# Optimization experiments

Measured on AMD Instinct MI355X. Metric: run time of the kernel, lower is better.

The kernel has to match this reference:

```python
import jax, jax.numpy as jnp
import numpy as np

L, H, C, HS, V, BS = 4, 8, 512, 64, 32000, 2048  # layers, heads, n_embd, head_size, vocab, block_size
B, T = 2, 2048


def _ln(x, g, b, eps=1e-5):
    m = jnp.mean(x, axis=-1, keepdims=True)
    v = jnp.var(x, axis=-1, keepdims=True)
    return (x - m) * jax.lax.rsqrt(v + eps) * g + b


def setup_inputs() -> dict:
    key = jax.random.key(0)
    ks = jax.random.split(key, 12)
    s = 0.02
    f = jnp.float32
    return {
        "idx": jax.random.randint(ks[0], (B, T), 0, V),
        "tok_emb": jax.random.normal(ks[1], (V, C), f) * s,
        "pos_emb": jax.random.normal(ks[2], (BS, C), f) * s,
        "ln1_g": jnp.ones((L, C), f), "ln1_b": jnp.zeros((L, C), f),
        "wq": jax.random.normal(ks[3], (L, H, C, HS), f) * s,
        "wk": jax.random.normal(ks[4], (L, H, C, HS), f) * s,
        "wv": jax.random.normal(ks[5], (L, H, C, HS), f) * s,
        "proj_w": jax.random.normal(ks[6], (L, C, C), f) * s,
        "proj_b": jnp.zeros((L, C), f),
        "ln2_g": jnp.ones((L, C), f), "ln2_b": jnp.zeros((L, C), f),
        "ff_w1": jax.random.normal(ks[7], (L, C, 4 * C), f) * s,
        "ff_b1": jnp.zeros((L, 4 * C), f),
        "ff_w2": jax.random.normal(ks[8], (L, 4 * C, C), f) * s,
        "ff_b2": jnp.zeros((L, C), f),
        "ffln_g": jnp.ones((L, C), f), "ffln_b": jnp.zeros((L, C), f),
        "lm_w": jax.random.normal(ks[9], (C, V), f) * s,
        "lm_b": jnp.zeros((V,), f),
    }


def reference(idx, tok_emb, pos_emb, ln1_g, ln1_b, wq, wk, wv, proj_w, proj_b,
              ln2_g, ln2_b, ff_w1, ff_b1, ff_w2, ff_b2, ffln_g, ffln_b, lm_w, lm_b):
    Tn = idx.shape[1]
    x = tok_emb[idx] + pos_emb[:Tn]  # [B,T,C]
    causal = jnp.tril(jnp.ones((Tn, Tn), bool))
    for l in range(L):
        h = _ln(x, ln1_g[l], ln1_b[l])
        q = jnp.einsum('btc,hcd->bhtd', h, wq[l])
        k = jnp.einsum('btc,hcd->bhtd', h, wk[l])
        v = jnp.einsum('btc,hcd->bhtd', h, wv[l])
        # NOTE: original module does NOT scale by 1/sqrt(head_size)
        wei = jnp.einsum('bhtd,bhsd->bhts', q, k)
        wei = jnp.where(causal, wei, -jnp.inf)
        wei = jax.nn.softmax(wei, axis=-1)
        att = jnp.einsum('bhts,bhsd->bhtd', wei, v)  # [B,H,T,HS]
        att = att.transpose(0, 2, 1, 3).reshape(x.shape[0], Tn, C)
        x = x + att @ proj_w[l].T + proj_b[l]
        h2 = _ln(x, ln2_g[l], ln2_b[l])
        ff = jax.nn.relu(h2 @ ff_w1[l] + ff_b1[l]) @ ff_w2[l] + ff_b2[l]
        ff = _ln(ff, ffln_g[l], ffln_b[l])  # FeedForward has trailing LayerNorm
        x = x + ff
    logits = x @ lm_w + lm_b  # [B,T,V]
    return logits
```

## Files before the change

kernel.cpp:

```cpp
#include <hip/hip_runtime.h>
#include <math.h>

#define NLAYER 4
#define NH     8
#define CDIM   512
#define HS     64
#define VOCAB  32000
#define BB     2
#define TT     2048
#define MROWS  (BB*TT)
#define QKVW   (3*CDIM)
#define NHEADS (BB*NH)

typedef __attribute__((ext_vector_type(8))) short bf16x8;
typedef __attribute__((ext_vector_type(4))) float f32x4;

__device__ __forceinline__ unsigned short f2bf(float f) {
    unsigned int u = __float_as_uint(f);
    u += 0x7FFF + ((u >> 16) & 1);
    return (unsigned short)(u >> 16);
}

#define GLOAD16(g, l) __builtin_amdgcn_global_load_lds( \
    (const __attribute__((address_space(1))) void*)(g), \
    (__attribute__((address_space(3))) void*)(l), 16, 0, 0)

template<int FLAGS, bool OUTBF>
__global__ __launch_bounds__(256) void mfma_gemm(
    const unsigned short* __restrict__ A, int lda,
    const unsigned short* __restrict__ Bt, int ldb,
    const float* __restrict__ bias,
    void* __restrict__ Cout, int ldc,
    const float* __restrict__ resid,
    int K)
{
    __shared__ unsigned short As[128*64];
    __shared__ unsigned short Bs[128*64];
    const int tid = threadIdx.x;
    const int w = tid >> 6, l = tid & 63;
    const int wr = w >> 1, wc = w & 1;
    const long m0 = (long)blockIdx.y * 128;
    const long n0 = (long)blockIdx.x * 128;
    const int srow = l >> 3;
    const int scol = (l & 7) << 3;
    const unsigned short* Ab = A + m0*lda;
    const unsigned short* Bb = Bt + n0*ldb;
    const int fr = l & 15;
    const int fk = (l >> 4) << 3;

    f32x4 acc[4][4];
    #pragma unroll
    for (int m = 0; m < 4; m++)
        #pragma unroll
        for (int n = 0; n < 4; n++) acc[m][n] = (f32x4)0.0f;

    for (int k0 = 0; k0 < K; k0 += 64) {
        __syncthreads();
        #pragma unroll
        for (int i = 0; i < 4; i++) {
            int seg = w*4 + i;
            GLOAD16(Ab + (long)(seg*8 + srow)*lda + k0 + scol, As + seg*512);
            GLOAD16(Bb + (long)(seg*8 + srow)*ldb + k0 + scol, Bs + seg*512);
        }
        __syncthreads();
        #pragma unroll
        for (int kk = 0; kk < 2; kk++) {
            bf16x8 af[4], bf[4];
            #pragma unroll
            for (int m = 0; m < 4; m++)
                af[m] = *(const bf16x8*)&As[(wr*64 + m*16 + fr)*64 + kk*32 + fk];
            #pragma unroll
            for (int n = 0; n < 4; n++)
                bf[n] = *(const bf16x8*)&Bs[(wc*64 + n*16 + fr)*64 + kk*32 + fk];
            #pragma unroll
            for (int m = 0; m < 4; m++)
                #pragma unroll
                for (int n = 0; n < 4; n++)
                    acc[m][n] = __builtin_amdgcn_mfma_f32_16x16x32_bf16(
                        af[m], bf[n], acc[m][n], 0, 0, 0);
        }
    }

    const int rg = (l >> 4) << 2;
    #pragma unroll
    for (int n = 0; n < 4; n++) {
        long gn = n0 + wc*64 + n*16 + fr;
        float bv = (FLAGS & 1) ? bias[gn] : 0.f;
        #pragma unroll
        for (int m = 0; m < 4; m++) {
            #pragma unroll
            for (int r = 0; r < 4; r++) {
                long gm = m0 + wr*64 + m*16 + rg + r;
                float val = acc[m][n][r] + bv;
                if (FLAGS & 2) val = fmaxf(val, 0.f);
                if (FLAGS & 4) val += resid[gm*ldc + gn];
                if (OUTBF) ((unsigned short*)Cout)[gm*ldc + gn] = f2bf(val);
                else       ((float*)Cout)[gm*ldc + gn] = val;
            }
        }
    }
}

__global__ __launch_bounds__(256) void mfma_gemm_qkv(
    const unsigned short* __restrict__ A,
    const unsigned short* __restrict__ Bt,
    unsigned short* __restrict__ qh,
    unsigned short* __restrict__ kh,
    unsigned short* __restrict__ vt)
{
    __shared__ unsigned short As[128*64];
    __shared__ unsigned short Bs[128*64];
    const int tid = threadIdx.x;
    const int w = tid >> 6, l = tid & 63;
    const int wr = w >> 1, wc = w & 1;
    const long m0 = (long)blockIdx.y * 128;
    const long n0 = (long)blockIdx.x * 128;
    const int srow = l >> 3;
    const int scol = (l & 7) << 3;
    const unsigned short* Ab = A + m0*CDIM;
    const unsigned short* Bb = Bt + n0*CDIM;
    const int fr = l & 15;
    const int fk = (l >> 4) << 3;

    f32x4 acc[4][4];
    #pragma unroll
    for (int m = 0; m < 4; m++)
        #pragma unroll
        for (int n = 0; n < 4; n++) acc[m][n] = (f32x4)0.0f;

    for (int k0 = 0; k0 < CDIM; k0 += 64) {
        __syncthreads();
        #pragma unroll
        for (int i = 0; i < 4; i++) {
            int seg = w*4 + i;
            GLOAD16(Ab + (long)(seg*8 + srow)*CDIM + k0 + scol, As + seg*512);
            GLOAD16(Bb + (long)(seg*8 + srow)*CDIM + k0 + scol, Bs + seg*512);
        }
        __syncthreads();
        #pragma unroll
        for (int kk = 0; kk < 2; kk++) {
            bf16x8 af[4], bf[4];
            #pragma unroll
            for (int m = 0; m < 4; m++)
                af[m] = *(const bf16x8*)&As[(wr*64 + m*16 + fr)*64 + kk*32 + fk];
            #pragma unroll
            for (int n = 0; n < 4; n++)
                bf[n] = *(const bf16x8*)&Bs[(wc*64 + n*16 + fr)*64 + kk*32 + fk];
            #pragma unroll
            for (int m = 0; m < 4; m++)
                #pragma unroll
                for (int n = 0; n < 4; n++)
                    acc[m][n] = __builtin_amdgcn_mfma_f32_16x16x32_bf16(
                        af[m], bf[n], acc[m][n], 0, 0, 0);
        }
    }

    const int rg = (l >> 4) << 2;
    #pragma unroll
    for (int n = 0; n < 4; n++) {
        int gn = (int)(n0 + wc*64 + n*16 + fr);
        int which = gn >> 9, hh = (gn >> 6) & 7, d = gn & 63;
        #pragma unroll
        for (int m = 0; m < 4; m++) {
            #pragma unroll
            for (int r = 0; r < 4; r++) {
                int gm = (int)(m0 + wr*64 + m*16 + rg + r);
                int b = gm >> 11, t = gm & (TT-1);
                int head = b*NH + hh;
                unsigned short val = f2bf(acc[m][n][r]);
                if (which == 0)      qh[((long)head*TT + t)*HS + d] = val;
                else if (which == 1) kh[((long)head*TT + t)*HS + d] = val;
                else                 vt[((long)head*HS + d)*TT + t] = val;
            }
        }
    }
}

__global__ __launch_bounds__(256) void attn_part(
    const unsigned short* __restrict__ qh,
    const unsigned short* __restrict__ kh,
    const unsigned short* __restrict__ vt,
    float* __restrict__ oP, float* __restrict__ ml)
{
    __shared__ unsigned short Ks[2][64*64];
    __shared__ unsigned short Vts[2][64*64];
    __shared__ unsigned short Ps[4][32*72];
    const int tid = threadIdx.x;
    const int w = tid >> 6, l = tid & 63;
    const int fr = l & 15, g = l >> 4;
    const int head = blockIdx.y;
    const int sp = blockIdx.z;
    const int x = blockIdx.x;
    const int qt0 = x * 128;
    const int qw = qt0 + w*32;
    const unsigned short* Qb = qh + (long)head*TT*HS;
    const unsigned short* Kb = kh + (long)head*TT*HS;
    const unsigned short* Vb = vt + (long)head*HS*TT;

    bf16x8 aq[2][2];
    #pragma unroll
    for (int mt = 0; mt < 2; mt++)
        #pragma unroll
        for (int ks = 0; ks < 2; ks++)
            aq[mt][ks] = *(const bf16x8*)&Qb[(long)(qw + mt*16 + fr)*HS + ks*32 + g*8];

    f32x4 acc_o[2][4];
    float mrun[2][4], lsum[2][4];
    #pragma unroll
    for (int mt = 0; mt < 2; mt++) {
        #pragma unroll
        for (int r = 0; r < 4; r++) { mrun[mt][r] = -INFINITY; lsum[mt][r] = 0.f; }
        #pragma unroll
        for (int n = 0; n < 4; n++) acc_o[mt][n] = (f32x4)0.0f;
    }

    const int cbeg = sp * (x + 1);
    const int cend = cbeg + (x + 1);
    const int srow = l >> 3;
    const int scol = ((l & 7) ^ (srow & 7)) << 3;

    auto stage = [&](int c) {
        int buf = c & 1;
        int s0_ = c*64;
        #pragma unroll
        for (int i = 0; i < 2; i++) {
            int rb = i*32 + w*8;
            GLOAD16(Kb + (long)(s0_ + rb + srow)*HS + scol, &Ks[buf][rb*64]);
            GLOAD16(Vb + (long)(rb + srow)*TT + s0_ + scol, &Vts[buf][rb*64]);
        }
    };

    stage(cbeg);
    for (int c = cbeg; c < cend; c++) {
        const int s0 = c*64;
        const int buf = c & 1;
        __syncthreads();
        if (c + 1 < cend) stage(c+1);
        if (s0 > qw + 31) continue;

        bf16x8 bk[4][2];
        #pragma unroll
        for (int n = 0; n < 4; n++)
            #pragma unroll
            for (int ks = 0; ks < 2; ks++) {
                int row = n*16 + fr;
                int u = (ks*4 + g) ^ (row & 7);
                bk[n][ks] = *(const bf16x8*)&Ks[buf][row*64 + u*8];
            }
        f32x4 sc[2][4];
        #pragma unroll
        for (int mt = 0; mt < 2; mt++)
            #pragma unroll
            for (int n = 0; n < 4; n++) sc[mt][n] = (f32x4)0.0f;
        #pragma unroll
        for (int ks = 0; ks < 2; ks++)
            #pragma unroll
            for (int mt = 0; mt < 2; mt++)
                #pragma unroll
                for (int n = 0; n < 4; n++)
                    sc[mt][n] = __builtin_amdgcn_mfma_f32_16x16x32_bf16(
                        aq[mt][ks], bk[n][ks], sc[mt][n], 0, 0, 0);

        #pragma unroll
        for (int mt = 0; mt < 2; mt++) {
            #pragma unroll
            for (int r = 0; r < 4; r++) {
                int q = qw + mt*16 + g*4 + r;
                float rmax = -INFINITY;
                #pragma unroll
                for (int n = 0; n < 4; n++) {
                    float v = sc[mt][n][r];
                    v = (s0 + n*16 + fr <= q) ? v : -INFINITY;
                    sc[mt][n][r] = v;
                    rmax = fmaxf(rmax, v);
                }
                #pragma unroll
                for (int off = 8; off >= 1; off >>= 1)
                    rmax = fmaxf(rmax, __shfl_xor(rmax, off));
                float mnew = fmaxf(mrun[mt][r], rmax);
                float scale = __expf(mrun[mt][r] - mnew);
                float ps = 0.f;
                #pragma unroll
                for (int n = 0; n < 4; n++) {
                    float p = __expf(sc[mt][n][r] - mnew);
                    sc[mt][n][r] = p;
                    ps += p;
                }
                #pragma unroll
                for (int off = 8; off >= 1; off >>= 1)
                    ps += __shfl_xor(ps, off);
                lsum[mt][r] = lsum[mt][r]*scale + ps;
                mrun[mt][r] = mnew;
                #pragma unroll
                for (int n = 0; n < 4; n++) acc_o[mt][n][r] *= scale;
            }
        }

        #pragma unroll
        for (int mt = 0; mt < 2; mt++)
            #pragma unroll
            for (int n = 0; n < 4; n++)
                #pragma unroll
                for (int r = 0; r < 4; r++)
                    Ps[w][(mt*16 + g*4 + r)*72 + n*16 + fr] = f2bf(sc[mt][n][r]);

        bf16x8 ap[2][2], bv[4][2];
        #pragma unroll
        for (int mt = 0; mt < 2; mt++)
            #pragma unroll
            for (int ks = 0; ks < 2; ks++)
                ap[mt][ks] = *(const bf16x8*)&Ps[w][(mt*16 + fr)*72 + ks*32 + g*8];
        #pragma unroll
        for (int n = 0; n < 4; n++)
            #pragma unroll
            for (int ks = 0; ks < 2; ks++) {
                int row = n*16 + fr;
                int u = (ks*4 + g) ^ (row & 7);
                bv[n][ks] = *(const bf16x8*)&Vts[buf][row*64 + u*8];
            }
        #pragma unroll
        for (int ks = 0; ks < 2; ks++)
            #pragma unroll
            for (int mt = 0; mt < 2; mt++)
                #pragma unroll
                for (int n = 0; n < 4; n++)
                    acc_o[mt][n] = __builtin_amdgcn_mfma_f32_16x16x32_bf16(
                        ap[mt][ks], bv[n][ks], acc_o[mt][n], 0, 0, 0);
    }

    float* oB = oP + ((long)(head*2 + sp)*TT)*HS;
    float* mlB = ml + ((long)(head*2 + sp)*TT)*2;
    #pragma unroll
    for (int mt = 0; mt < 2; mt++) {
        #pragma unroll
        for (int n = 0; n < 4; n++)
            #pragma unroll
            for (int r = 0; r < 4; r++)
                oB[(long)(qw + mt*16 + g*4 + r)*HS + n*16 + fr] = acc_o[mt][n][r];
        if (fr == 0) {
            #pragma unroll
            for (int r = 0; r < 4; r++) {
                int t = qw + mt*16 + g*4 + r;
                mlB[t*2]     = mrun[mt][r];
                mlB[t*2 + 1] = lsum[mt][r];
            }
        }
    }
}

__global__ __launch_bounds__(256) void attn_combine(
    const float* __restrict__ oP, const float* __restrict__ ml,
    unsigned short* __restrict__ att)
{
    const int gid = blockIdx.x*4 + (threadIdx.x >> 6);
    const int lane = threadIdx.x & 63;
    const int head = gid >> 11, t = gid & (TT-1);
    const int b = head >> 3, hh = head & 7;
    const long i0 = (long)(head*2 + 0)*TT + t;
    const long i1 = (long)(head*2 + 1)*TT + t;
    const float m0 = ml[i0*2], l0 = ml[i0*2+1];
    const float m1 = ml[i1*2], l1 = ml[i1*2+1];
    const float M = fmaxf(m0, m1);
    const float e0 = __expf(m0 - M), e1 = __expf(m1 - M);
    const float L = l0*e0 + l1*e1;
    const float v = (oP[i0*HS + lane]*e0 + oP[i1*HS + lane]*e1) / L;
    att[((long)b*TT + t)*CDIM + hh*HS + lane] = f2bf(v);
}

__global__ __launch_bounds__(256) void transpose_cast(
    const float* __restrict__ in, unsigned short* __restrict__ out,
    int R, int Cn, long in_z1, long in_z2, long out_z1, long out_z2, int z2n)
{
    const int z = blockIdx.z;
    const int z1 = z / z2n, z2 = z % z2n;
    const float* ip = in + (long)z1*in_z1 + (long)z2*in_z2;
    unsigned short* op = out + (long)z1*out_z1 + (long)z2*out_z2;
    __shared__ float tile[32][33];
    const int tx = threadIdx.x & 31, ty = threadIdx.x >> 5;
    const long r0 = (long)blockIdx.y*32, c0 = (long)blockIdx.x*32;
    #pragma unroll
    for (int i = 0; i < 4; i++)
        tile[ty + i*8][tx] = ip[(r0 + ty + i*8)*Cn + c0 + tx];
    __syncthreads();
    #pragma unroll
    for (int i = 0; i < 4; i++)
        op[(c0 + ty + i*8)*R + r0 + tx] = f2bf(tile[tx][ty + i*8]);
}

__global__ __launch_bounds__(256) void cast_kernel(
    const float* __restrict__ in, unsigned short* __restrict__ out, long n)
{
    long i = ((long)blockIdx.x*256 + threadIdx.x) * 4;
    if (i >= n) return;
    float4 v = *(const float4*)(in + i);
    ushort4 u = make_ushort4(f2bf(v.x), f2bf(v.y), f2bf(v.z), f2bf(v.w));
    *(ushort4*)(out + i) = u;
}

__global__ void embed_kernel(const int* __restrict__ idx,
                             const float* __restrict__ tok,
                             const float* __restrict__ pos,
                             float* __restrict__ x)
{
    const int r = blockIdx.x;
    const int t = r & (TT-1);
    const long tr = idx[r];
    const float* te = tok + tr*CDIM;
    const float* pe = pos + (long)t*CDIM;
    float* xo = x + (long)r*CDIM;
    for (int c = threadIdx.x; c < CDIM; c += blockDim.x)
        xo[c] = te[c] + pe[c];
}

template<int MODE>
__global__ __launch_bounds__(256) void ln_kernel(
    const float* __restrict__ in, const float* __restrict__ g,
    const float* __restrict__ bb, void* __restrict__ outp,
    void* __restrict__ outp2)
{
    const int wave = threadIdx.x >> 6;
    const int lane = threadIdx.x & 63;
    const long r = (long)blockIdx.x*4 + wave;
    const float* xr = in + r*CDIM;
    float vals[8];
    float s = 0.f;
    #pragma unroll
    for (int i = 0; i < 8; i++) { vals[i] = xr[lane + i*64]; s += vals[i]; }
    #pragma unroll
    for (int o = 32; o >= 1; o >>= 1) s += __shfl_xor(s, o);
    const float mean = s * (1.f/CDIM);
    float vs = 0.f;
    #pragma unroll
    for (int i = 0; i < 8; i++) { float d = vals[i]-mean; vs += d*d; }
    #pragma unroll
    for (int o = 32; o >= 1; o >>= 1) vs += __shfl_xor(vs, o);
    const float rstd = rsqrtf(vs*(1.f/CDIM) + 1e-5f);
    #pragma unroll
    for (int i = 0; i < 8; i++) {
        int c = lane + i*64;
        float nv = (vals[i]-mean)*rstd*g[c] + bb[c];
        if (MODE == 1) {
            ((unsigned short*)outp)[r*CDIM + c] = f2bf(nv);
        } else {
            float s2 = ((float*)outp)[r*CDIM + c] + nv;
            ((float*)outp)[r*CDIM + c] = s2;
            if (MODE == 3) ((unsigned short*)outp2)[r*CDIM + c] = f2bf(s2);
        }
    }
}

extern "C" void kernel_launch(void* const* d_in, const int* in_sizes, int n_in,
                              void* d_out, int out_size, void* d_ws, size_t ws_size,
                              hipStream_t stream)
{
    const int*   idx   = (const int*)  d_in[0];
    const float* tok   = (const float*)d_in[1];
    const float* pos   = (const float*)d_in[2];
    const float* ln1g  = (const float*)d_in[3];
    const float* ln1b  = (const float*)d_in[4];
    const float* wq    = (const float*)d_in[5];
    const float* wk    = (const float*)d_in[6];
    const float* wv    = (const float*)d_in[7];
    const float* projw = (const float*)d_in[8];
    const float* projb = (const float*)d_in[9];
    const float* ln2g  = (const float*)d_in[10];
    const float* ln2b  = (const float*)d_in[11];
    const float* ffw1  = (const float*)d_in[12];
    const float* ffb1  = (const float*)d_in[13];
    const float* ffw2  = (const float*)d_in[14];
    const float* ffb2  = (const float*)d_in[15];
    const float* flng  = (const float*)d_in[16];
    const float* flnb  = (const float*)d_in[17];
    const float* lmw   = (const float*)d_in[18];
    const float* lmb   = (const float*)d_in[19];
    float* out = (float*)d_out;

    char* wp = (char*)d_ws;
    float* x  = (float*)wp;           wp += (size_t)MROWS*CDIM*4;
    float* ff = (float*)wp;           wp += (size_t)MROWS*CDIM*4;
    unsigned short* h     = (unsigned short*)wp; wp += (size_t)MROWS*CDIM*2;
    unsigned short* lmt   = (unsigned short*)wp; wp += (size_t)VOCAB*CDIM*2;
    unsigned short* ff1t  = (unsigned short*)wp; wp += (size_t)NLAYER*4*CDIM*CDIM*2;
    unsigned short* ff2t  = (unsigned short*)wp; wp += (size_t)NLAYER*4*CDIM*CDIM*2;
    unsigned short* qkvt  = (unsigned short*)wp; wp += (size_t)NLAYER*QKVW*CDIM*2;
    unsigned short* projc = (unsigned short*)wp; wp += (size_t)NLAYER*CDIM*CDIM*2;
    unsigned short* qh    = (unsigned short*)wp; wp += (size_t)NHEADS*TT*HS*2;
    unsigned short* kh    = (unsigned short*)wp; wp += (size_t)NHEADS*TT*HS*2;
    unsigned short* vt    = (unsigned short*)wp; wp += (size_t)NHEADS*TT*HS*2;

    unsigned short* f1  = (unsigned short*)d_out;
    unsigned short* att = f1 + (size_t)MROWS*4*CDIM;
    float* oP = (float*)(att + (size_t)MROWS*CDIM);
    float* ml = oP + (size_t)NHEADS*2*TT*HS;

    transpose_cast<<<dim3(VOCAB/32, CDIM/32, 1), 256, 0, stream>>>(
        lmw, lmt, CDIM, VOCAB, 0, 0, 0, 0, 1);
    transpose_cast<<<dim3(4*CDIM/32, CDIM/32, NLAYER), 256, 0, stream>>>(
        ffw1, ff1t, CDIM, 4*CDIM, (long)CDIM*4*CDIM, 0, (long)4*CDIM*CDIM, 0, 1);
    transpose_cast<<<dim3(CDIM/32, 4*CDIM/32, NLAYER), 256, 0, stream>>>(
        ffw2, ff2t, 4*CDIM, CDIM, (long)4*CDIM*CDIM, 0, (long)CDIM*4*CDIM, 0, 1);
    {
        const size_t QBLK = (size_t)CDIM * CDIM;
        transpose_cast<<<dim3(HS/32, CDIM/32, NLAYER*NH), 256, 0, stream>>>(
            wq, qkvt,            CDIM, HS,
            (long)NH*CDIM*HS, (long)CDIM*HS, (long)QKVW*CDIM, (long)HS*CDIM, NH);
        transpose_cast<<<dim3(HS/32, CDIM/32, NLAYER*NH), 256, 0, stream>>>(
            wk, qkvt + QBLK,     CDIM, HS,
            (long)NH*CDIM*HS, (long)CDIM*HS, (long)QKVW*CDIM, (long)HS*CDIM, NH);
        transpose_cast<<<dim3(HS/32, CDIM/32, NLAYER*NH), 256, 0, stream>>>(
            wv, qkvt + 2*QBLK,   CDIM, HS,
            (long)NH*CDIM*HS, (long)CDIM*HS, (long)QKVW*CDIM, (long)HS*CDIM, NH);
    }
    cast_kernel<<<(NLAYER*CDIM*CDIM/4 + 255)/256, 256, 0, stream>>>(
        projw, projc, (long)NLAYER*CDIM*CDIM);

    embed_kernel<<<MROWS, 256, 0, stream>>>(idx, tok, pos, x);

    for (int l = 0; l < NLAYER; l++) {
        const unsigned short* qkvt_l = qkvt + (size_t)l*QKVW*CDIM;
        const unsigned short* projc_l = projc + (size_t)l*CDIM*CDIM;
        const unsigned short* ff1t_l = ff1t + (size_t)l*4*CDIM*CDIM;
        const unsigned short* ff2t_l = ff2t + (size_t)l*4*CDIM*CDIM;

        ln_kernel<1><<<MROWS/4, 256, 0, stream>>>(x, ln1g + l*CDIM, ln1b + l*CDIM, h, nullptr);

        mfma_gemm_qkv<<<dim3(QKVW/128, MROWS/128), 256, 0, stream>>>(
            h, qkvt_l, qh, kh, vt);

        attn_part<<<dim3(TT/128, NHEADS, 2), 256, 0, stream>>>(qh, kh, vt, oP, ml);
        attn_combine<<<dim3(NHEADS*TT/4), 256, 0, stream>>>(oP, ml, att);

        mfma_gemm<5,false><<<dim3(CDIM/128, MROWS/128), 256, 0, stream>>>(
            att, CDIM, projc_l, CDIM, projb + l*CDIM, x, CDIM, x, CDIM);

        ln_kernel<1><<<MROWS/4, 256, 0, stream>>>(x, ln2g + l*CDIM, ln2b + l*CDIM, h, nullptr);

        mfma_gemm<3,true><<<dim3(4*CDIM/128, MROWS/128), 256, 0, stream>>>(
            h, CDIM, ff1t_l, CDIM, ffb1 + (size_t)l*4*CDIM, f1, 4*CDIM, nullptr, CDIM);

        mfma_gemm<1,false><<<dim3(CDIM/128, MROWS/128), 256, 0, stream>>>(
            f1, 4*CDIM, ff2t_l, 4*CDIM, ffb2 + l*CDIM, ff, CDIM, nullptr, 4*CDIM);

        if (l == NLAYER-1)
            ln_kernel<3><<<MROWS/4, 256, 0, stream>>>(ff, flng + l*CDIM, flnb + l*CDIM, x, h);
        else
            ln_kernel<2><<<MROWS/4, 256, 0, stream>>>(ff, flng + l*CDIM, flnb + l*CDIM, x, nullptr);
    }

    mfma_gemm<1,false><<<dim3(VOCAB/128, MROWS/128), 256, 0, stream>>>(
        h, CDIM, lmt, CDIM, lmb, out, VOCAB, nullptr, CDIM);
}
```

Measured before the change: 1.034 ms.

## Double-buffer GEMM LDS tiles with XOR swizzle, grouped LM-head tiling, nontemporal stores

The GEMM kernels now double-buffer the LDS tiles, so the next K-slice loads while MFMAs run on the current one. The LDS layout gets an XOR swizzle to cut bank conflicts. The LM-head GEMM uses a swizzled block order and nontemporal stores for its large fp32 logits output, aiming at better L2 reuse of weight tiles and less cache pollution. The attention split count is now a macro, and the combine kernel is generalized to loop over it. Double buffering doubles LDS use to 64KB per block, which may lower occupancy.

```diff
diff --git a/kernel.cpp b/kernel.cpp
--- a/kernel.cpp
+++ b/kernel.cpp
@@ -11,6 +11,7 @@
 #define MROWS  (BB*TT)
 #define QKVW   (3*CDIM)
 #define NHEADS (BB*NH)
+#define ASPLIT 2
 
 typedef __attribute__((ext_vector_type(8))) short bf16x8;
 typedef __attribute__((ext_vector_type(4))) float f32x4;
@@ -25,7 +26,9 @@
     (const __attribute__((address_space(1))) void*)(g), \
     (__attribute__((address_space(3))) void*)(l), 16, 0, 0)
 
-template<int FLAGS, bool OUTBF>
+#define SWZ(row, chunk) (((row)*64) + ((((chunk) ^ ((row)&7)))*8))
+
+template<int FLAGS, bool OUTBF, bool MSWIZ>
 __global__ __launch_bounds__(256) void mfma_gemm(
     const unsigned short* __restrict__ A, int lda,
     const unsigned short* __restrict__ Bt, int ldb,
@@ -34,19 +37,118 @@
     const float* __restrict__ resid,
     int K)
 {
-    __shared__ unsigned short As[128*64];
-    __shared__ unsigned short Bs[128*64];
+    __shared__ unsigned short As[2][128*64];
+    __shared__ unsigned short Bs[2][128*64];
+    const int tid = threadIdx.x;
+    const int w = tid >> 6, l = tid & 63;
+    const int wr = w >> 1, wc = w & 1;
+    long m0, n0;
+    if (MSWIZ) {
+        const int mt = gridDim.x;
+        const int flat = blockIdx.y * mt + blockIdx.x;
+        const int cpx = (mt * gridDim.y) >> 3;
+        const int swz = (flat & 7) * cpx + (flat >> 3);
+        m0 = (long)(swz % mt) * 128;
+        n0 = (long)(swz / mt) * 128;
+    } else {
+        m0 = (long)blockIdx.y * 128;
+        n0 = (long)blockIdx.x * 128;
+    }
+    const int srow = l >> 3;
+    const int scol = ((l & 7) ^ (srow & 7)) << 3;
+    const unsigned short* Ab = A + m0*lda;
+    const unsigned short* Bb = Bt + n0*ldb;
+    const int fr = l & 15;
+    const int g  = l >> 4;
+
+    f32x4 acc[4][4];
+    #pragma unroll
+    for (int m = 0; m < 4; m++)
+        #pragma unroll
+        for (int n = 0; n < 4; n++) acc[m][n] = (f32x4)0.0f;
+
+    auto stage = [&](int k0, int buf) {
+        #pragma unroll
+        for (int i = 0; i < 4; i++) {
+            int seg = w*4 + i;
+            GLOAD16(Ab + (long)(seg*8 + srow)*lda + k0 + scol, &As[buf][seg*512]);
+            GLOAD16(Bb + (long)(seg*8 + srow)*ldb + k0 + scol, &Bs[buf][seg*512]);
+        }
+    };
+
+    const int nk = K >> 6;
+    stage(0, 0);
+    for (int ks = 0; ks < nk; ks++) {
+        const int buf = ks & 1;
+        __syncthreads();
+        if (ks + 1 < nk) stage((ks+1) << 6, buf ^ 1);
+        #pragma unroll
+        for (int kk = 0; kk < 2; kk++) {
+            bf16x8 af[4], bf[4];
+            #pragma unroll
+            for (int m = 0; m < 4; m++) {
+                int row = wr*64 + m*16 + fr;
+                af[m] = *(const bf16x8*)&As[buf][SWZ(row, kk*4 + g)];
+            }
+            #pragma unroll
+            for (int n = 0; n < 4; n++) {
+                int row = wc*64 + n*16 + fr;
+                bf[n] = *(const bf16x8*)&Bs[buf][SWZ(row, kk*4 + g)];
+            }
+            #pragma unroll
+            for (int m = 0; m < 4; m++)
+                #pragma unroll
+                for (int n = 0; n < 4; n++)
+                    acc[m][n] = __builtin_amdgcn_mfma_f32_16x16x32_bf16(
+                        af[m], bf[n], acc[m][n], 0, 0, 0);
+        }
+    }
+
+    const int rg = g << 2;
+    #pragma unroll
+    for (int n = 0; n < 4; n++) {
+        long gn = n0 + wc*64 + n*16 + fr;
+        float bv = (FLAGS & 1) ? bias[gn] : 0.f;
+        #pragma unroll
+        for (int m = 0; m < 4; m++) {
+            #pragma unroll
+            for (int r = 0; r < 4; r++) {
+                long gm = m0 + wr*64 + m*16 + rg + r;
+                float val = acc[m][n][r] + bv;
+                if (FLAGS & 2) val = fmaxf(val, 0.f);
+                if (FLAGS & 4) val += resid[gm*ldc + gn];
+                if (OUTBF) {
+                    ((unsigned short*)Cout)[gm*ldc + gn] = f2bf(val);
+                } else if (FLAGS & 8) {
+                    __builtin_nontemporal_store(val, &((float*)Cout)[gm*ldc + gn]);
+                } else {
+                    ((float*)Cout)[gm*ldc + gn] = val;
+                }
+            }
+        }
+    }
+}
+
+__global__ __launch_bounds__(256) void mfma_gemm_qkv(
+    const unsigned short* __restrict__ A,
+    const unsigned short* __restrict__ Bt,
+    unsigned short* __restrict__ qh,
+    unsigned short* __restrict__ kh,
+    unsigned short* __restrict__ vt)
+{
+    __shared__ unsigned short As[2][128*64];
+    __shared__ unsigned short Bs[2][128*64];
     const int tid = threadIdx.x;
     const int w = tid >> 6, l = tid & 63;
     const int wr = w >> 1, wc = w & 1;
     const long m0 = (long)blockIdx.y * 128;
     const long n0 = (long)blockIdx.x * 128;
     const int srow = l >> 3;
-    const int scol = (l & 7) << 3;
-    const unsigned short* Ab = A + m0*lda;
-    const unsigned short* Bb = Bt + n0*ldb;
+    const int scol = ((l & 7) ^ (srow & 7)) << 3;
+    const unsigned short* Ab = A + m0*CDIM;
+    const unsigned short* Bb = Bt + n0*CDIM;
     const int fr = l & 15;
-    const int fk = (l >> 4) << 3;
+    const int g  = l >> 4;
 
     f32x4 acc[4][4];
     #pragma unroll
@@ -54,24 +156,34 @@
         #pragma unroll
         for (int n = 0; n < 4; n++) acc[m][n] = (f32x4)0.0f;
 
-    for (int k0 = 0; k0 < K; k0 += 64) {
-        __syncthreads();
+    auto stage = [&](int k0, int buf) {
         #pragma unroll
         for (int i = 0; i < 4; i++) {
             int seg = w*4 + i;
-            GLOAD16(Ab + (long)(seg*8 + srow)*lda + k0 + scol, As + seg*512);
-            GLOAD16(Bb + (long)(seg*8 + srow)*ldb + k0 + scol, Bs + seg*512);
-        }
+            GLOAD16(Ab + (long)(seg*8 + srow)*CDIM + k0 + scol, &As[buf][seg*512]);
+            GLOAD16(Bb + (long)(seg*8 + srow)*CDIM + k0 + scol, &Bs[buf][seg*512]);
+        }
+    };
+
+    const int nk = CDIM >> 6;
+    stage(0, 0);
+    for (int ks = 0; ks < nk; ks++) {
+        const int buf = ks & 1;
         __syncthreads();
+        if (ks + 1 < nk) stage((ks+1) << 6, buf ^ 1);
         #pragma unroll
         for (int kk = 0; kk < 2; kk++) {
             bf16x8 af[4], bf[4];
             #pragma unroll
-            for (int m = 0; m < 4; m++)
-                af[m] = *(const bf16x8*)&As[(wr*64 + m*16 + fr)*64 + kk*32 + fk];
-            #pragma unroll
-            for (int n = 0; n < 4; n++)
-                bf[n] = *(const bf16x8*)&Bs[(wc*64 + n*16 + fr)*64 + kk*32 + fk];
+            for (int m = 0; m < 4; m++) {
+                int row = wr*64 + m*16 + fr;
+                af[m] = *(const bf16x8*)&As[buf][SWZ(row, kk*4 + g)];
+            }
+            #pragma unroll
+            for (int n = 0; n < 4; n++) {
+                int row = wc*64 + n*16 + fr;
+                bf[n] = *(const bf16x8*)&Bs[buf][SWZ(row, kk*4 + g)];
+            }
             #pragma unroll
             for (int m = 0; m < 4; m++)
                 #pragma unroll
@@ -81,81 +193,7 @@
         }
     }
 
-    const int rg = (l >> 4) << 2;
-    #pragma unroll
-    for (int n = 0; n < 4; n++) {
-        long gn = n0 + wc*64 + n*16 + fr;
-        float bv = (FLAGS & 1) ? bias[gn] : 0.f;
-        #pragma unroll
-        for (int m = 0; m < 4; m++) {
-            #pragma unroll
-            for (int r = 0; r < 4; r++) {
-                long gm = m0 + wr*64 + m*16 + rg + r;
-                float val = acc[m][n][r] + bv;
-                if (FLAGS & 2) val = fmaxf(val, 0.f);
-                if (FLAGS & 4) val += resid[gm*ldc + gn];
-                if (OUTBF) ((unsigned short*)Cout)[gm*ldc + gn] = f2bf(val);
-                else       ((float*)Cout)[gm*ldc + gn] = val;
-            }
-        }
-    }
-}
-
-__global__ __launch_bounds__(256) void mfma_gemm_qkv(
-    const unsigned short* __restrict__ A,
-    const unsigned short* __restrict__ Bt,
-    unsigned short* __restrict__ qh,
-    unsigned short* __restrict__ kh,
-    unsigned short* __restrict__ vt)
-{
-    __shared__ unsigned short As[128*64];
-    __shared__ unsigned short Bs[128*64];
-    const int tid = threadIdx.x;
-    const int w = tid >> 6, l = tid & 63;
-    const int wr = w >> 1, wc = w & 1;
-    const long m0 = (long)blockIdx.y * 128;
-    const long n0 = (long)blockIdx.x * 128;
-    const int srow = l >> 3;
-    const int scol = (l & 7) << 3;
-    const unsigned short* Ab = A + m0*CDIM;
-    const unsigned short* Bb = Bt + n0*CDIM;
-    const int fr = l & 15;
-    const int fk = (l >> 4) << 3;
-
-    f32x4 acc[4][4];
-    #pragma unroll
-    for (int m = 0; m < 4; m++)
-        #pragma unroll
-        for (int n = 0; n < 4; n++) acc[m][n] = (f32x4)0.0f;
-
-    for (int k0 = 0; k0 < CDIM; k0 += 64) {
-        __syncthreads();
-        #pragma unroll
-        for (int i = 0; i < 4; i++) {
-            int seg = w*4 + i;
-            GLOAD16(Ab + (long)(seg*8 + srow)*CDIM + k0 + scol, As + seg*512);
-            GLOAD16(Bb + (long)(seg*8 + srow)*CDIM + k0 + scol, Bs + seg*512);
-        }
-        __syncthreads();
-        #pragma unroll
-        for (int kk = 0; kk < 2; kk++) {
-            bf16x8 af[4], bf[4];
-            #pragma unroll
-            for (int m = 0; m < 4; m++)
-                af[m] = *(const bf16x8*)&As[(wr*64 + m*16 + fr)*64 + kk*32 + fk];
-            #pragma unroll
-            for (int n = 0; n < 4; n++)
-                bf[n] = *(const bf16x8*)&Bs[(wc*64 + n*16 + fr)*64 + kk*32 + fk];
-            #pragma unroll
-            for (int m = 0; m < 4; m++)
-                #pragma unroll
-                for (int n = 0; n < 4; n++)
-                    acc[m][n] = __builtin_amdgcn_mfma_f32_16x16x32_bf16(
-                        af[m], bf[n], acc[m][n], 0, 0, 0);
-        }
-    }
-
-    const int rg = (l >> 4) << 2;
+    const int rg = g << 2;
     #pragma unroll
     for (int n = 0; n < 4; n++) {
         int gn = (int)(n0 + wc*64 + n*16 + fr);
@@ -191,8 +229,7 @@
     const int head = blockIdx.y;
     const int sp = blockIdx.z;
     const int x = blockIdx.x;
-    const int qt0 = x * 128;
-    const int qw = qt0 + w*32;
+    const int qw = x*128 + w*32;
     const unsigned short* Qb = qh + (long)head*TT*HS;
     const unsigned short* Kb = kh + (long)head*TT*HS;
     const unsigned short* Vb = vt + (long)head*HS*TT;
@@ -244,8 +281,7 @@
             #pragma unroll
             for (int ks = 0; ks < 2; ks++) {
                 int row = n*16 + fr;
-                int u = (ks*4 + g) ^ (row & 7);
-                bk[n][ks] = *(const bf16x8*)&Ks[buf][row*64 + u*8];
+                bk[n][ks] = *(const bf16x8*)&Ks[buf][SWZ(row, ks*4 + g)];
             }
         f32x4 sc[2][4];
         #pragma unroll
@@ -315,8 +351,7 @@
             #pragma unroll
             for (int ks = 0; ks < 2; ks++) {
                 int row = n*16 + fr;
-                int u = (ks*4 + g) ^ (row & 7);
-                bv[n][ks] = *(const bf16x8*)&Vts[buf][row*64 + u*8];
+                bv[n][ks] = *(const bf16x8*)&Vts[buf][SWZ(row, ks*4 + g)];
             }
         #pragma unroll
         for (int ks = 0; ks < 2; ks++)
@@ -328,8 +363,8 @@
                         ap[mt][ks], bv[n][ks], acc_o[mt][n], 0, 0, 0);
     }
 
-    float* oB = oP + ((long)(head*2 + sp)*TT)*HS;
-    float* mlB = ml + ((long)(head*2 + sp)*TT)*2;
+    float* oB = oP + ((long)(head*ASPLIT + sp)*TT)*HS;
+    float* mlB = ml + ((long)(head*ASPLIT + sp)*TT)*2;
     #pragma unroll
     for (int mt = 0; mt < 2; mt++) {
         #pragma unroll
@@ -356,15 +391,22 @@
     const int lane = threadIdx.x & 63;
     const int head = gid >> 11, t = gid & (TT-1);
     const int b = head >> 3, hh = head & 7;
-    const long i0 = (long)(head*2 + 0)*TT + t;
-    const long i1 = (long)(head*2 + 1)*TT + t;
-    const float m0 = ml[i0*2], l0 = ml[i0*2+1];
-    const float m1 = ml[i1*2], l1 = ml[i1*2+1];
-    const float M = fmaxf(m0, m1);
-    const float e0 = __expf(m0 - M), e1 = __expf(m1 - M);
-    const float L = l0*e0 + l1*e1;
-    const float v = (oP[i0*HS + lane]*e0 + oP[i1*HS + lane]*e1) / L;
-    att[((long)b*TT + t)*CDIM + hh*HS + lane] = f2bf(v);
+    float m[ASPLIT], lv[ASPLIT];
+    float M = -INFINITY;
+    #pragma unroll
+    for (int s = 0; s < ASPLIT; s++) {
+        long i = (long)(head*ASPLIT + s)*TT + t;
+        m[s] = ml[i*2]; lv[s] = ml[i*2+1];
+        M = fmaxf(M, m[s]);
+    }
+    float L = 0.f, v = 0.f;
+    #pragma unroll
+    for (int s = 0; s < ASPLIT; s++) {
+        float e = __expf(m[s] - M);
+        L += lv[s]*e;
+        v += oP[((long)(head*ASPLIT + s)*TT + t)*HS + lane]*e;
+    }
+    att[((long)b*TT + t)*CDIM + hh*HS + lane] = f2bf(v / L);
 }
 
 __global__ __launch_bounds__(256) void transpose_cast(
@@ -491,7 +533,7 @@
     unsigned short* f1  = (unsigned short*)d_out;
     unsigned short* att = f1 + (size_t)MROWS*4*CDIM;
     float* oP = (float*)(att + (size_t)MROWS*CDIM);
-    float* ml = oP + (size_t)NHEADS*2*TT*HS;
+    float* ml = oP + (size_t)NHEADS*ASPLIT*TT*HS;
 
     transpose_cast<<<dim3(VOCAB/32, CDIM/32, 1), 256, 0, stream>>>(
         lmw, lmt, CDIM, VOCAB, 0, 0, 0, 0, 1);
@@ -527,18 +569,18 @@
         mfma_gemm_qkv<<<dim3(QKVW/128, MROWS/128), 256, 0, stream>>>(
             h, qkvt_l, qh, kh, vt);
 
-        attn_part<<<dim3(TT/128, NHEADS, 2), 256, 0, stream>>>(qh, kh, vt, oP, ml);
+        attn_part<<<dim3(TT/128, NHEADS, ASPLIT), 256, 0, stream>>>(qh, kh, vt, oP, ml);
         attn_combine<<<dim3(NHEADS*TT/4), 256, 0, stream>>>(oP, ml, att);
 
-        mfma_gemm<5,false><<<dim3(CDIM/128, MROWS/128), 256, 0, stream>>>(
+        mfma_gemm<5,false,false><<<dim3(CDIM/128, MROWS/128), 256, 0, stream>>>(
             att, CDIM, projc_l, CDIM, projb + l*CDIM, x, CDIM, x, CDIM);
 
         ln_kernel<1><<<MROWS/4, 256, 0, stream>>>(x, ln2g + l*CDIM, ln2b + l*CDIM, h, nullptr);
 
-        mfma_gemm<3,true><<<dim3(4*CDIM/128, MROWS/128), 256, 0, stream>>>(
+        mfma_gemm<3,true,false><<<dim3(4*CDIM/128, MROWS/128), 256, 0, stream>>>(
             h, CDIM, ff1t_l, CDIM, ffb1 + (size_t)l*4*CDIM, f1, 4*CDIM, nullptr, CDIM);
 
-        mfma_gemm<1,false><<<dim3(CDIM/128, MROWS/128), 256, 0, stream>>>(
+        mfma_gemm<1,false,false><<<dim3(CDIM/128, MROWS/128), 256, 0, stream>>>(
             f1, 4*CDIM, ff2t_l, 4*CDIM, ffb2 + l*CDIM, ff, CDIM, nullptr, 4*CDIM);
 
         if (l == NLAYER-1)
@@ -547,6 +589,6 @@
             ln_kernel<2><<<MROWS/4, 256, 0, stream>>>(ff, flng + l*CDIM, flnb + l*CDIM, x, nullptr);
     }
 
-    mfma_gemm<1,false><<<dim3(VOCAB/128, MROWS/128), 256, 0, stream>>>(
+    mfma_gemm<9,false,true><<<dim3(MROWS/128, VOCAB/128), 256, 0, stream>>>(
         h, CDIM, lmt, CDIM, lmb, out, VOCAB, nullptr, CDIM);
 }
```

Result: faster. 935.9 us (-9.5%).
